# Kernel optimization log

Hardware: AMD Instinct MI355X
Metric: run time of the kernel (lower is better)

The kernel has to match this reference:

```python
import jax, jax.numpy as jnp
import numpy as np

CHUNK = 256
HEADS = 8  # kr
EPS = 1e-6


def setup_inputs() -> dict:
    key = jax.random.key(0)
    ks = jax.random.split(key, 8)
    B, S, D, V, K = 2, 4096, 1024, 32000, 128
    s = 0.02
    return {
        "x": jax.random.randint(ks[0], (B, S), 0, V),
        "emb_table": jax.random.normal(ks[1], (V, D), dtype=jnp.float32) * s,
        "Wq": jax.random.normal(ks[2], (D, K), dtype=jnp.float32) * s,
        "Wk": jax.random.normal(ks[3], (D, K), dtype=jnp.float32) * s,
        "Wv": jax.random.normal(ks[4], (D, D), dtype=jnp.float32) * s,
        "Wo": jax.random.normal(ks[5], (D, D), dtype=jnp.float32) * s,
        "ln_g": jnp.ones((D,), jnp.float32),
        "ln_b": jnp.zeros((D,), jnp.float32),
        "out_W": jax.random.normal(ks[6], (D, V), dtype=jnp.float32) * s,
        "out_b": jnp.zeros((V,), jnp.float32),
    }


def _forward(x, emb_table, Wq, Wk, Wv, Wo, ln_g, ln_b, out_W, out_b):
    B, S = x.shape
    D = emb_table.shape[1]
    K = Wq.shape[1]
    H, C = HEADS, CHUNK
    dk, dv = K // H, D // H
    nC = S // C

    emb = emb_table[x]                                   # [B,S,D]
    # build_causal_context: sum of emb shifted by 0..3
    ctx = emb
    for o in (1, 2, 3):
        ctx = ctx + jnp.pad(emb, ((0, 0), (o, 0), (0, 0)))[:, :S, :]

    phi = lambda t: jax.nn.elu(t) + 1.0                  # positive feature map
    q = phi(ctx @ Wq).reshape(B, nC, C, H, dk)
    k = phi(ctx @ Wk).reshape(B, nC, C, H, dk)
    v = (ctx @ Wv).reshape(B, nC, C, H, dv)
    xc = ctx.reshape(B, nC, C, D)

    qs, ks_, vs, xs = (jnp.moveaxis(a, 1, 0) for a in (q, k, v, xc))
    mask = jnp.tril(jnp.ones((C, C), bool))

    def step(carry, inp):
        S_st, S_t, bk, bv = carry                        # S_st:[B,H,dk,dv], S_t:[B,H,dk]
        qc, kc, vc, cc = inp
        # intra-chunk causal attention
        att = jnp.einsum('bchk,bshk->bhcs', qc, kc)
        att = jnp.where(mask[None, None], att, 0.0)
        num = jnp.einsum('bhcs,bshv->bchv', att, vc)
        # exact attention over previous chunk (bypass_kv)
        byp = jnp.einsum('bchk,bshk->bhcs', qc, bk)
        num = num + jnp.einsum('bhcs,bshv->bchv', byp, bv)
        # older chunks via outer-product state S_prev
        num = num + jnp.einsum('bchk,bhkv->bchv', qc, S_st)
        # denominator: running key-sum (S_time) + prev-chunk keys + causal cumsum
        kcum = jnp.cumsum(kc, axis=1)
        den = (jnp.einsum('bchk,bchk->bch', qc, kcum)
               + jnp.einsum('bchk,bhk->bch', qc, S_t + bk.sum(axis=1)))
        o = num / (den[..., None] + EPS)
        o = o.reshape(o.shape[0], C, D) @ Wo + cc        # out proj + residual
        # fold previous chunk into the long-range state, current chunk becomes bypass
        S_new = S_st + jnp.einsum('bshk,bshv->bhkv', bk, bv)
        St_new = S_t + bk.sum(axis=1)
        return (S_new, St_new, kc, vc), o

    init = (jnp.zeros((B, H, dk, dv), ctx.dtype),
            jnp.zeros((B, H, dk), ctx.dtype),
            jnp.zeros((B, C, H, dk), ctx.dtype),
            jnp.zeros((B, C, H, dv), ctx.dtype))
    _, outs = jax.lax.scan(step, init, (qs, ks_, vs, xs))
    out = jnp.moveaxis(outs, 0, 1).reshape(B, S, D)

    mu = out.mean(-1, keepdims=True)
    var = out.var(-1, keepdims=True)
    out = (out - mu) * jax.lax.rsqrt(var + 1e-5) * ln_g + ln_b
    return out @ out_W + out_b                           # [B,S,V] logits


def reference(x, emb_table, Wq, Wk, Wv, Wo, ln_g, ln_b, out_W, out_b):
    return _forward(x, emb_table, Wq, Wk, Wv, Wo, ln_g, ln_b, out_W, out_b)
```

## Files before the change

kernel.cpp:

```cpp
#include <hip/hip_runtime.h>
#include <hip/hip_bf16.h>

typedef __bf16 bf16_t;
typedef __bf16 bf16x4 __attribute__((ext_vector_type(4)));
typedef __bf16 bf16x8 __attribute__((ext_vector_type(8)));
typedef float f32x4 __attribute__((ext_vector_type(4)));

#define BB 2
#define SS 4096
#define DD 1024
#define VV 32000
#define HH 8
#define CC 256
#define NC 16

#define GLD_LDS16(gp, lp) __builtin_amdgcn_global_load_lds( \
    (const __attribute__((address_space(1))) void*)(gp),    \
    (__attribute__((address_space(3))) void*)(lp), 16, 0, 0)

__global__ __launch_bounds__(256) void ctx_kernel(
    const int* __restrict__ x, const float* __restrict__ emb,
    bf16_t* __restrict__ ctxb)
{
  const int row = blockIdx.x;
  const int b = row >> 12, s = row & (SS - 1);
  const int t = threadIdx.x;
  float4 a = make_float4(0.f, 0.f, 0.f, 0.f);
  #pragma unroll
  for (int o = 0; o < 4; ++o) {
    if (s - o >= 0) {
      const int idx = x[b * SS + s - o];
      const float4 e = *(const float4*)(emb + (size_t)idx * DD + t * 4);
      a.x += e.x; a.y += e.y; a.z += e.z; a.w += e.w;
    }
  }
  bf16x4 bv;
  bv[0] = (__bf16)a.x; bv[1] = (__bf16)a.y; bv[2] = (__bf16)a.z; bv[3] = (__bf16)a.w;
  *(bf16x4*)(ctxb + (size_t)row * DD + t * 4) = bv;
}

__global__ __launch_bounds__(256) void transpose_cvt(
    const float* __restrict__ src, bf16_t* __restrict__ dst,
    int srcRows, int srcCols)
{
  __shared__ __align__(16) float tile[128][65];
  const int c0 = blockIdx.x * 64, r0 = blockIdx.y * 128;
  const int t = threadIdx.x;
  #pragma unroll
  for (int p = 0; p < 8; ++p) {
    const int r = p * 16 + (t >> 4);
    const int c = (t & 15) * 4;
    *(float4*)&tile[r][c] = *(const float4*)(src + (size_t)(r0 + r) * srcCols + c0 + c);
  }
  __syncthreads();
  #pragma unroll
  for (int p = 0; p < 4; ++p) {
    const int j = p * 16 + (t >> 4);
    const int i0 = (t & 15) * 8;
    bf16x8 v;
    #pragma unroll
    for (int e = 0; e < 8; ++e) v[e] = (__bf16)tile[i0 + e][j];
    *(bf16x8*)(dst + (size_t)(c0 + j) * srcRows + r0 + i0) = v;
  }
}

template<int EPI>
__global__ __launch_bounds__(256, 4) void gemm128_kernel(
    const bf16_t* __restrict__ A, const bf16_t* __restrict__ BT,
    float* __restrict__ C, bf16_t* __restrict__ Cb,
    const float* __restrict__ extraF, const bf16_t* __restrict__ extraB,
    bf16_t* __restrict__ qb, bf16_t* __restrict__ kbx, bf16_t* __restrict__ vtb,
    int N, int K)
{
  __shared__ __align__(16) bf16_t As[128 * 64];
  __shared__ __align__(16) bf16_t Bs[128 * 64];
  const int bid = blockIdx.x;
  const int i = bid >> 3, xcd = bid & 7;
  const int by = xcd * 8 + (i & 7);
  const int bx = i >> 3;
  const int n0 = bx * 128, m0 = by * 128;
  const int t = threadIdx.x;
  const int w = t >> 6, lane = t & 63;
  const int wm = (w >> 1) * 64, wn = (w & 1) * 64;
  const int lr = lane & 15, lq = lane >> 4;
  f32x4 acc[4][4] = {};

  for (int k0 = 0; k0 < K; k0 += 64) {
    #pragma unroll
    for (int j = 0; j < 4; ++j) {
      const int idx = j * 256 + t;
      const int r = idx >> 3;
      const int sc = ((idx & 7) ^ (r & 7)) * 8;
      GLD_LDS16(A  + (size_t)(m0 + r) * K + k0 + sc, As + (size_t)idx * 8);
      GLD_LDS16(BT + (size_t)(n0 + r) * K + k0 + sc, Bs + (size_t)idx * 8);
    }
    asm volatile("s_waitcnt vmcnt(0)" ::: "memory");
    __syncthreads();
    bf16x8 af[4][2], bfr[4][2];
    #pragma unroll
    for (int ii = 0; ii < 4; ++ii) {
      const int ra = wm + ii * 16 + lr;
      const int rb = wn + ii * 16 + lr;
      #pragma unroll
      for (int ks = 0; ks < 2; ++ks) {
        const int col = ((ks * 4 + lq) ^ (lr & 7)) * 8;
        af[ii][ks]  = *(const bf16x8*)(As + ra * 64 + col);
        bfr[ii][ks] = *(const bf16x8*)(Bs + rb * 64 + col);
      }
    }
    #pragma unroll
    for (int mi = 0; mi < 4; ++mi)
      #pragma unroll
      for (int ni = 0; ni < 4; ++ni) {
        acc[mi][ni] = __builtin_amdgcn_mfma_f32_16x16x32_bf16(af[mi][0], bfr[ni][0], acc[mi][ni], 0, 0, 0);
        acc[mi][ni] = __builtin_amdgcn_mfma_f32_16x16x32_bf16(af[mi][1], bfr[ni][1], acc[mi][ni], 0, 0, 0);
      }
    __syncthreads();
  }

  if (EPI == 3) {
    #pragma unroll
    for (int mi = 0; mi < 4; ++mi) {
      const int row0 = m0 + wm + mi * 16 + lq * 4;
      #pragma unroll
      for (int ni = 0; ni < 4; ++ni) {
        const int col = n0 + wn + ni * 16 + lr;
        if (col < 256) {
          #pragma unroll
          for (int r = 0; r < 4; ++r) {
            float v = acc[mi][ni][r];
            v = v > 0.f ? v + 1.f : __expf(v);
            if (col < 128) qb [(size_t)(row0 + r) * 128 + col      ] = (__bf16)v;
            else           kbx[(size_t)(row0 + r) * 128 + col - 128] = (__bf16)v;
          }
        } else {
          const int vcol = col - 256;
          const int hh = vcol >> 7, dv = vcol & 127;
          const int bb = row0 >> 12, s0 = row0 & (SS - 1);
          bf16x4 pv;
          #pragma unroll
          for (int r = 0; r < 4; ++r) pv[r] = (__bf16)acc[mi][ni][r];
          *(bf16x4*)(vtb + ((size_t)((bb * HH + hh) * 128 + dv)) * SS + s0) = pv;
        }
      }
    }
    return;
  }
  #pragma unroll
  for (int mi = 0; mi < 4; ++mi) {
    #pragma unroll
    for (int r = 0; r < 4; ++r) {
      const int row = m0 + wm + mi * 16 + lq * 4 + r;
      #pragma unroll
      for (int ni = 0; ni < 4; ++ni) {
        const int col = n0 + wn + ni * 16 + lr;
        float v = acc[mi][ni][r];
        if (EPI == 1) {
          v += extraF[col];
          __builtin_nontemporal_store(v, &C[(size_t)row * N + col]);
        }
        if (EPI == 2) {
          v += (float)extraB[(size_t)row * N + col];
          Cb[(size_t)row * N + col] = (__bf16)v;
        }
      }
    }
  }
}

__global__ __launch_bounds__(64) void gstate_kernel(
    const bf16_t* __restrict__ kb, const bf16_t* __restrict__ vT,
    float* __restrict__ G, float* __restrict__ KS)
{
  const int bid = blockIdx.x;
  const int h = bid & 7, c = (bid >> 3) & 15, b = bid >> 7;
  const int lane = threadIdx.x;
  const int lr = lane & 15, lq = lane >> 4;
  __shared__ __align__(16) bf16_t ktl[16][264];
  for (int ss = 0; ss < 4; ++ss) {
    const int s = ss * 64 + lane;
    const bf16_t* src = kb + (size_t)(b * SS + c * CC + s) * 128 + h * 16;
    const bf16x8 v0 = *(const bf16x8*)src;
    const bf16x8 v1 = *(const bf16x8*)(src + 8);
    #pragma unroll
    for (int ii = 0; ii < 8; ++ii) { ktl[ii][s] = v0[ii]; ktl[8 + ii][s] = v1[ii]; }
  }
  __syncthreads();
  if (lane < 16) {
    float ks = 0.f;
    for (int s = 0; s < 256; ++s) ks += (float)ktl[lane][s];
    KS[((size_t)((b * NC + c) * HH + h)) * 16 + lane] = ks;
  }
  bf16x8 af[8];
  #pragma unroll
  for (int sk = 0; sk < 8; ++sk)
    af[sk] = *(const bf16x8*)&ktl[lr][sk * 32 + lq * 8];
  float* gout = G + ((size_t)((b * NC + c) * HH + h)) * 2048;
  #pragma unroll
  for (int nf = 0; nf < 8; ++nf) {
    f32x4 acc = {0.f, 0.f, 0.f, 0.f};
    #pragma unroll
    for (int sk = 0; sk < 8; ++sk) {
      const bf16x8 vb = *(const bf16x8*)(vT +
          ((size_t)((b * HH + h) * 128 + nf * 16 + lr)) * SS + c * CC + sk * 32 + lq * 8);
      acc = __builtin_amdgcn_mfma_f32_16x16x32_bf16(af[sk], vb, acc, 0, 0, 0);
    }
    #pragma unroll
    for (int r = 0; r < 4; ++r)
      gout[(size_t)(lq * 4 + r) * 128 + nf * 16 + lr] = acc[r];
  }
}

__global__ __launch_bounds__(512, 2) void attn_kernel(
    const bf16_t* __restrict__ qb, const bf16_t* __restrict__ kb,
    const bf16_t* __restrict__ vT, const float* __restrict__ Gb,
    const float* __restrict__ KS, bf16_t* __restrict__ outp)
{
  const int bid = blockIdx.x;
  const int h = bid & 7, c = (bid >> 3) & 15, b = bid >> 7;
  const int t = threadIdx.x;
  const int w = t >> 6, lane = t & 63;
  const int lr = lane & 15, lq = lane >> 4;
  const int rowbase = b * SS + c * CC;

  __shared__ __align__(16) bf16_t q_lds[256][24];
  __shared__ __align__(16) bf16_t k_lds[512][24];
  __shared__ __align__(16) bf16_t vt_lds[128][72];
  __shared__ __align__(16) bf16_t p_lds[8][32][72];
  __shared__ float s_f32[16][128];
  __shared__ float z_lds[16];
  __shared__ float dstate[256];

  if (t < 256) {
    const bf16_t* src = qb + (size_t)(rowbase + t) * 128 + h * 16;
    *(uint4*)&q_lds[t][0] = *(const uint4*)src;
    *(uint4*)&q_lds[t][8] = *(const uint4*)(src + 8);
  }
  {
    if (t < 256 && c == 0) {
      const uint4 z = {0u, 0u, 0u, 0u};
      *(uint4*)&k_lds[t][0] = z; *(uint4*)&k_lds[t][8] = z;
    } else {
      const int sg = (t < 256) ? (c - 1) * CC + t : c * CC + (t - 256);
      const bf16_t* src = kb + (size_t)(b * SS + sg) * 128 + h * 16;
      *(uint4*)&k_lds[t][0] = *(const uint4*)src;
      *(uint4*)&k_lds[t][8] = *(const uint4*)(src + 8);
    }
  }
  if (t < 16) {
    float z = 0.f;
    for (int j = 0; j + 2 <= c; ++j) z += KS[((size_t)((b * NC + j) * HH + h)) * 16 + t];
    z_lds[t] = z;
  }
  if (c >= 2) {
    for (int idx = t; idx < 2048; idx += 512) {
      float sv = 0.f;
      for (int j = 0; j + 2 <= c; ++j)
        sv += Gb[((size_t)((b * NC + j) * HH + h)) * 2048 + idx];
      ((float*)s_f32)[idx] = sv;
    }
  }
  __syncthreads();
  if (t < 256) {
    float d = 0.f;
    #pragma unroll
    for (int ii = 0; ii < 16; ++ii) d += (float)q_lds[t][ii] * z_lds[ii];
    dstate[t] = d;
  }

  const int wrow = w * 32;
  bf16x8 qf[2];
  #pragma unroll
  for (int mi = 0; mi < 2; ++mi) {
    bf16x8 v = {};
    if (lq < 2) v = *(const bf16x8*)&q_lds[wrow + mi * 16 + lr][lq * 8];
    qf[mi] = v;
  }
  f32x4 acc[2][8] = {};
  float den_l[2][4] = {};
  const int nc0 = (c == 0) ? 4 : 0;

  for (int nc = nc0; nc < 8; ++nc) {
    __syncthreads();
    {
      const int dv = t >> 2, kk = (t & 3) * 16;
      const int key0 = nc * 64;
      const int sg = (key0 < 256) ? (c - 1) * CC + key0 : c * CC + key0 - 256;
      const bf16_t* src = vT + ((size_t)((b * HH + h) * 128 + dv)) * SS + sg + kk;
      *(uint4*)&vt_lds[dv][kk]     = *(const uint4*)src;
      *(uint4*)&vt_lds[dv][kk + 8] = *(const uint4*)(src + 8);
    }
    __syncthreads();
    f32x4 attf[2][4];
    #pragma unroll
    for (int nf = 0; nf < 4; ++nf) {
      bf16x8 kv = {};
      if (lq < 2) kv = *(const bf16x8*)&k_lds[nc * 64 + nf * 16 + lr][lq * 8];
      #pragma unroll
      for (int mi = 0; mi < 2; ++mi) {
        const f32x4 zero = {0.f, 0.f, 0.f, 0.f};
        attf[mi][nf] = __builtin_amdgcn_mfma_f32_16x16x32_bf16(qf[mi], kv, zero, 0, 0, 0);
      }
    }
    #pragma unroll
    for (int mi = 0; mi < 2; ++mi)
      #pragma unroll
      for (int nf = 0; nf < 4; ++nf)
        #pragma unroll
        for (int r = 0; r < 4; ++r) {
          const int row_l = wrow + mi * 16 + lq * 4 + r;
          const int key_l = nc * 64 + nf * 16 + lr;
          float a = attf[mi][nf][r];
          if (key_l >= 256 && key_l - 256 > row_l) a = 0.f;
          den_l[mi][r] += a;
          p_lds[w][mi * 16 + lq * 4 + r][nf * 16 + lr] = (__bf16)a;
        }
    #pragma unroll
    for (int ks = 0; ks < 2; ++ks) {
      bf16x8 pa[2];
      #pragma unroll
      for (int mi = 0; mi < 2; ++mi)
        pa[mi] = *(const bf16x8*)&p_lds[w][mi * 16 + lr][ks * 32 + lq * 8];
      #pragma unroll
      for (int nf = 0; nf < 8; ++nf) {
        const bf16x8 vb = *(const bf16x8*)&vt_lds[nf * 16 + lr][ks * 32 + lq * 8];
        #pragma unroll
        for (int mi = 0; mi < 2; ++mi)
          acc[mi][nf] = __builtin_amdgcn_mfma_f32_16x16x32_bf16(pa[mi], vb, acc[mi][nf], 0, 0, 0);
      }
    }
  }

  if (c >= 2) {
    #pragma unroll
    for (int mi = 0; mi < 2; ++mi)
      for (int r = 0; r < 4; ++r) {
        const int row_l = wrow + mi * 16 + lq * 4 + r;
        float qrow[16];
        #pragma unroll
        for (int ii = 0; ii < 16; ++ii) qrow[ii] = (float)q_lds[row_l][ii];
        #pragma unroll
        for (int nf = 0; nf < 8; ++nf) {
          float sacc = 0.f;
          #pragma unroll
          for (int ii = 0; ii < 16; ++ii) sacc += qrow[ii] * s_f32[ii][nf * 16 + lr];
          acc[mi][nf][r] += sacc;
        }
      }
  }
  #pragma unroll
  for (int mi = 0; mi < 2; ++mi)
    #pragma unroll
    for (int r = 0; r < 4; ++r) {
      float d = den_l[mi][r];
      d += __shfl_xor(d, 1, 64); d += __shfl_xor(d, 2, 64);
      d += __shfl_xor(d, 4, 64); d += __shfl_xor(d, 8, 64);
      const int row_l = wrow + mi * 16 + lq * 4 + r;
      den_l[mi][r] = 1.0f / (d + dstate[row_l] + 1e-6f);
    }
  #pragma unroll
  for (int mi = 0; mi < 2; ++mi)
    #pragma unroll
    for (int r = 0; r < 4; ++r) {
      const size_t row_g = rowbase + wrow + mi * 16 + lq * 4 + r;
      const float inv = den_l[mi][r];
      #pragma unroll
      for (int nf = 0; nf < 8; ++nf)
        outp[row_g * DD + h * 128 + nf * 16 + lr] = (__bf16)(acc[mi][nf][r] * inv);
    }
}

__global__ __launch_bounds__(256) void ln_kernel(
    const bf16_t* __restrict__ hb, const float* __restrict__ g,
    const float* __restrict__ bta, bf16_t* __restrict__ out)
{
  const int row = blockIdx.x;
  const int t = threadIdx.x;
  const bf16x4 xb = *(const bf16x4*)(hb + (size_t)row * DD + t * 4);
  float4 x = make_float4((float)xb[0], (float)xb[1], (float)xb[2], (float)xb[3]);
  float s  = x.x + x.y + x.z + x.w;
  float s2 = x.x*x.x + x.y*x.y + x.z*x.z + x.w*x.w;
  #pragma unroll
  for (int off = 32; off > 0; off >>= 1) {
    s  += __shfl_down(s,  off, 64);
    s2 += __shfl_down(s2, off, 64);
  }
  __shared__ float ws[8];
  if ((t & 63) == 0) { ws[(t >> 6) * 2] = s; ws[(t >> 6) * 2 + 1] = s2; }
  __syncthreads();
  const float ts  = ws[0] + ws[2] + ws[4] + ws[6];
  const float ts2 = ws[1] + ws[3] + ws[5] + ws[7];
  const float mu  = ts * (1.0f / DD);
  const float var = ts2 * (1.0f / DD) - mu * mu;
  const float inv = rsqrtf(var + 1e-5f);
  const float4 gv = ((const float4*)g)[t];
  const float4 bv = ((const float4*)bta)[t];
  bf16x4 o;
  o[0] = (__bf16)((x.x - mu) * inv * gv.x + bv.x);
  o[1] = (__bf16)((x.y - mu) * inv * gv.y + bv.y);
  o[2] = (__bf16)((x.z - mu) * inv * gv.z + bv.z);
  o[3] = (__bf16)((x.w - mu) * inv * gv.w + bv.w);
  *(bf16x4*)(out + (size_t)row * DD + t * 4) = o;
}

extern "C" void kernel_launch(void* const* d_in, const int* in_sizes, int n_in,
                              void* d_out, int out_size, void* d_ws, size_t ws_size,
                              hipStream_t stream) {
  (void)in_sizes; (void)n_in; (void)out_size; (void)ws_size;
  const int*   x    = (const int*)d_in[0];
  const float* emb  = (const float*)d_in[1];
  const float* Wq   = (const float*)d_in[2];
  const float* Wk   = (const float*)d_in[3];
  const float* Wv   = (const float*)d_in[4];
  const float* Wo   = (const float*)d_in[5];
  const float* ln_g = (const float*)d_in[6];
  const float* ln_b = (const float*)d_in[7];
  const float* outW = (const float*)d_in[8];
  const float* outb = (const float*)d_in[9];
  float* out = (float*)d_out;

  char* ws = (char*)d_ws;
  bf16_t* ctx_bf  = (bf16_t*)(ws + 0);
  bf16_t* qbuf    = (bf16_t*)(ws + 16777216ull);
  bf16_t* kbuf    = (bf16_t*)(ws + 18874368ull);
  bf16_t* vTbuf   = (bf16_t*)(ws + 20971520ull);
  bf16_t* attn_bf = (bf16_t*)(ws + 37748736ull);
  bf16_t* h_pre   = (bf16_t*)(ws + 54525952ull);
  float*  Gbuf    = (float*) (ws + 71303168ull);
  float*  KSbuf   = (float*) (ws + 73400320ull);
  bf16_t* WqkvT   = (bf16_t*)(ws + 73416704ull);
  bf16_t* WoT     = (bf16_t*)(ws + 76038144ull);
  bf16_t* outWT   = (bf16_t*)(ws + 78135296ull);
  bf16_t* h_bf    = attn_bf;

  transpose_cvt<<<dim3(2, 8),   256, 0, stream>>>(Wq,   WqkvT,             DD, 128);
  transpose_cvt<<<dim3(2, 8),   256, 0, stream>>>(Wk,   WqkvT + 128 * DD,  DD, 128);
  transpose_cvt<<<dim3(16, 8),  256, 0, stream>>>(Wv,   WqkvT + 256 * DD,  DD, DD);
  transpose_cvt<<<dim3(16, 8),  256, 0, stream>>>(Wo,   WoT,               DD, DD);
  transpose_cvt<<<dim3(500, 8), 256, 0, stream>>>(outW, outWT,             DD, VV);

  ctx_kernel<<<BB * SS, 256, 0, stream>>>(x, emb, ctx_bf);

  gemm128_kernel<3><<<(1280 / 128) * (BB * SS / 128), 256, 0, stream>>>(
      ctx_bf, WqkvT, nullptr, nullptr, nullptr, nullptr, qbuf, kbuf, vTbuf, 1280, DD);

  gstate_kernel<<<BB * NC * HH, 64, 0, stream>>>(kbuf, vTbuf, Gbuf, KSbuf);
  attn_kernel<<<BB * NC * HH, 512, 0, stream>>>(qbuf, kbuf, vTbuf, Gbuf, KSbuf, attn_bf);

  gemm128_kernel<2><<<(DD / 128) * (BB * SS / 128), 256, 0, stream>>>(
      attn_bf, WoT, nullptr, h_pre, nullptr, ctx_bf, nullptr, nullptr, nullptr, DD, DD);

  ln_kernel<<<BB * SS, 256, 0, stream>>>(h_pre, ln_g, ln_b, h_bf);

  gemm128_kernel<1><<<(VV / 128) * (BB * SS / 128), 256, 0, stream>>>(
      h_bf, outWT, out, nullptr, outb, nullptr, nullptr, nullptr, nullptr, VV, DD);
}
```

Measured before the change: 787.7 us.

## Make GEMM persistent over N tiles and prefetch next K-slice during MFMA

The GEMM kernel becomes persistent along N: each block owns one M tile and loops over N tiles with stride LANES, and the launch grid shrinks to 64*LANES blocks (1024 for the vocab projection). Fragments are read into registers, then the next K slice, or the first slice of the next N tile, is issued into LDS before the MFMAs run, so global loads overlap compute with a single LDS buffer. The intent is to hide load latency and cut block launch overhead. The cost is fewer resident blocks and possible tail imbalance, since 250 N tiles do not split evenly over 16 lanes.

```diff
diff --git a/kernel.cpp b/kernel.cpp
--- a/kernel.cpp
+++ b/kernel.cpp
@@ -64,104 +64,113 @@
   }
 }
 
+#define STAGE(N0S, K0S) do {                                                  \
+  _Pragma("unroll") for (int j = 0; j < 4; ++j) {                             \
+    const int idx = j * 256 + t;                                              \
+    const int r = idx >> 3;                                                   \
+    const int sc = ((idx & 7) ^ (r & 7)) * 8;                                 \
+    GLD_LDS16(A  + (size_t)(m0 + r) * K + (K0S) + sc, As + (size_t)idx * 8);  \
+    GLD_LDS16(BT + (size_t)((N0S) + r) * K + (K0S) + sc, Bs + (size_t)idx * 8); \
+  } } while (0)
+
 template<int EPI>
 __global__ __launch_bounds__(256, 4) void gemm128_kernel(
     const bf16_t* __restrict__ A, const bf16_t* __restrict__ BT,
     float* __restrict__ C, bf16_t* __restrict__ Cb,
     const float* __restrict__ extraF, const bf16_t* __restrict__ extraB,
     bf16_t* __restrict__ qb, bf16_t* __restrict__ kbx, bf16_t* __restrict__ vtb,
-    int N, int K)
+    int N, int K, int LANES)
 {
   __shared__ __align__(16) bf16_t As[128 * 64];
   __shared__ __align__(16) bf16_t Bs[128 * 64];
   const int bid = blockIdx.x;
-  const int i = bid >> 3, xcd = bid & 7;
-  const int by = xcd * 8 + (i & 7);
-  const int bx = i >> 3;
-  const int n0 = bx * 128, m0 = by * 128;
+  const int xcd = bid & 7, sl = (bid >> 3) & 7, lane16 = bid >> 6;
+  const int by = xcd * 8 + sl;
+  const int m0 = by * 128;
+  const int NBX = N >> 7;
   const int t = threadIdx.x;
   const int w = t >> 6, lane = t & 63;
   const int wm = (w >> 1) * 64, wn = (w & 1) * 64;
   const int lr = lane & 15, lq = lane >> 4;
-  f32x4 acc[4][4] = {};
-
-  for (int k0 = 0; k0 < K; k0 += 64) {
-    #pragma unroll
-    for (int j = 0; j < 4; ++j) {
-      const int idx = j * 256 + t;
-      const int r = idx >> 3;
-      const int sc = ((idx & 7) ^ (r & 7)) * 8;
-      GLD_LDS16(A  + (size_t)(m0 + r) * K + k0 + sc, As + (size_t)idx * 8);
-      GLD_LDS16(BT + (size_t)(n0 + r) * K + k0 + sc, Bs + (size_t)idx * 8);
-    }
-    asm volatile("s_waitcnt vmcnt(0)" ::: "memory");
-    __syncthreads();
-    bf16x8 af[4][2], bfr[4][2];
-    #pragma unroll
-    for (int ii = 0; ii < 4; ++ii) {
-      const int ra = wm + ii * 16 + lr;
-      const int rb = wn + ii * 16 + lr;
-      #pragma unroll
-      for (int ks = 0; ks < 2; ++ks) {
-        const int col = ((ks * 4 + lq) ^ (lr & 7)) * 8;
-        af[ii][ks]  = *(const bf16x8*)(As + ra * 64 + col);
-        bfr[ii][ks] = *(const bf16x8*)(Bs + rb * 64 + col);
-      }
-    }
-    #pragma unroll
-    for (int mi = 0; mi < 4; ++mi)
-      #pragma unroll
-      for (int ni = 0; ni < 4; ++ni) {
-        acc[mi][ni] = __builtin_amdgcn_mfma_f32_16x16x32_bf16(af[mi][0], bfr[ni][0], acc[mi][ni], 0, 0, 0);
-        acc[mi][ni] = __builtin_amdgcn_mfma_f32_16x16x32_bf16(af[mi][1], bfr[ni][1], acc[mi][ni], 0, 0, 0);
-      }
-    __syncthreads();
-  }
-
-  if (EPI == 3) {
-    #pragma unroll
-    for (int mi = 0; mi < 4; ++mi) {
-      const int row0 = m0 + wm + mi * 16 + lq * 4;
-      #pragma unroll
-      for (int ni = 0; ni < 4; ++ni) {
-        const int col = n0 + wn + ni * 16 + lr;
-        if (col < 256) {
+
+  STAGE(lane16 * 128, 0);
+
+  for (int bx = lane16; bx < NBX; bx += LANES) {
+    const int n0 = bx * 128;
+    f32x4 acc[4][4] = {};
+    for (int k0 = 0; k0 < K; k0 += 64) {
+      asm volatile("s_waitcnt vmcnt(0)" ::: "memory");
+      __syncthreads();
+      bf16x8 af[4][2], bfr[4][2];
+      #pragma unroll
+      for (int ii = 0; ii < 4; ++ii) {
+        const int ra = wm + ii * 16 + lr;
+        const int rb = wn + ii * 16 + lr;
+        #pragma unroll
+        for (int ks = 0; ks < 2; ++ks) {
+          const int col = ((ks * 4 + lq) ^ (lr & 7)) * 8;
+          af[ii][ks]  = *(const bf16x8*)(As + ra * 64 + col);
+          bfr[ii][ks] = *(const bf16x8*)(Bs + rb * 64 + col);
+        }
+      }
+      __syncthreads();
+      const int k1 = k0 + 64;
+      if (k1 < K)                STAGE(n0, k1);
+      else if (bx + LANES < NBX) STAGE((bx + LANES) * 128, 0);
+      #pragma unroll
+      for (int mi = 0; mi < 4; ++mi)
+        #pragma unroll
+        for (int ni = 0; ni < 4; ++ni) {
+          acc[mi][ni] = __builtin_amdgcn_mfma_f32_16x16x32_bf16(af[mi][0], bfr[ni][0], acc[mi][ni], 0, 0, 0);
+          acc[mi][ni] = __builtin_amdgcn_mfma_f32_16x16x32_bf16(af[mi][1], bfr[ni][1], acc[mi][ni], 0, 0, 0);
+        }
+    }
+
+    if (EPI == 3) {
+      #pragma unroll
+      for (int mi = 0; mi < 4; ++mi) {
+        const int row0 = m0 + wm + mi * 16 + lq * 4;
+        #pragma unroll
+        for (int ni = 0; ni < 4; ++ni) {
+          const int col = n0 + wn + ni * 16 + lr;
+          if (col < 256) {
+            #pragma unroll
+            for (int r = 0; r < 4; ++r) {
+              float v = acc[mi][ni][r];
+              v = v > 0.f ? v + 1.f : __expf(v);
+              if (col < 128) qb [(size_t)(row0 + r) * 128 + col      ] = (__bf16)v;
+              else           kbx[(size_t)(row0 + r) * 128 + col - 128] = (__bf16)v;
+            }
+          } else {
+            const int vcol = col - 256;
+            const int hh = vcol >> 7, dv = vcol & 127;
+            const int bb = row0 >> 12, s0 = row0 & (SS - 1);
+            bf16x4 pv;
+            #pragma unroll
+            for (int r = 0; r < 4; ++r) pv[r] = (__bf16)acc[mi][ni][r];
+            *(bf16x4*)(vtb + ((size_t)((bb * HH + hh) * 128 + dv)) * SS + s0) = pv;
+          }
+        }
+      }
+    } else {
+      #pragma unroll
+      for (int mi = 0; mi < 4; ++mi) {
+        #pragma unroll
+        for (int r = 0; r < 4; ++r) {
+          const int row = m0 + wm + mi * 16 + lq * 4 + r;
           #pragma unroll
-          for (int r = 0; r < 4; ++r) {
+          for (int ni = 0; ni < 4; ++ni) {
+            const int col = n0 + wn + ni * 16 + lr;
             float v = acc[mi][ni][r];
-            v = v > 0.f ? v + 1.f : __expf(v);
-            if (col < 128) qb [(size_t)(row0 + r) * 128 + col      ] = (__bf16)v;
-            else           kbx[(size_t)(row0 + r) * 128 + col - 128] = (__bf16)v;
+            if (EPI == 1) {
+              v += extraF[col];
+              __builtin_nontemporal_store(v, &C[(size_t)row * N + col]);
+            }
+            if (EPI == 2) {
+              v += (float)extraB[(size_t)row * N + col];
+              Cb[(size_t)row * N + col] = (__bf16)v;
+            }
           }
-        } else {
-          const int vcol = col - 256;
-          const int hh = vcol >> 7, dv = vcol & 127;
-          const int bb = row0 >> 12, s0 = row0 & (SS - 1);
-          bf16x4 pv;
-          #pragma unroll
-          for (int r = 0; r < 4; ++r) pv[r] = (__bf16)acc[mi][ni][r];
-          *(bf16x4*)(vtb + ((size_t)((bb * HH + hh) * 128 + dv)) * SS + s0) = pv;
-        }
-      }
-    }
-    return;
-  }
-  #pragma unroll
-  for (int mi = 0; mi < 4; ++mi) {
-    #pragma unroll
-    for (int r = 0; r < 4; ++r) {
-      const int row = m0 + wm + mi * 16 + lq * 4 + r;
-      #pragma unroll
-      for (int ni = 0; ni < 4; ++ni) {
-        const int col = n0 + wn + ni * 16 + lr;
-        float v = acc[mi][ni][r];
-        if (EPI == 1) {
-          v += extraF[col];
-          __builtin_nontemporal_store(v, &C[(size_t)row * N + col]);
-        }
-        if (EPI == 2) {
-          v += (float)extraB[(size_t)row * N + col];
-          Cb[(size_t)row * N + col] = (__bf16)v;
         }
       }
     }
@@ -441,17 +450,17 @@
 
   ctx_kernel<<<BB * SS, 256, 0, stream>>>(x, emb, ctx_bf);
 
-  gemm128_kernel<3><<<(1280 / 128) * (BB * SS / 128), 256, 0, stream>>>(
-      ctx_bf, WqkvT, nullptr, nullptr, nullptr, nullptr, qbuf, kbuf, vTbuf, 1280, DD);
+  gemm128_kernel<3><<<64 * 10, 256, 0, stream>>>(
+      ctx_bf, WqkvT, nullptr, nullptr, nullptr, nullptr, qbuf, kbuf, vTbuf, 1280, DD, 10);
 
   gstate_kernel<<<BB * NC * HH, 64, 0, stream>>>(kbuf, vTbuf, Gbuf, KSbuf);
   attn_kernel<<<BB * NC * HH, 512, 0, stream>>>(qbuf, kbuf, vTbuf, Gbuf, KSbuf, attn_bf);
 
-  gemm128_kernel<2><<<(DD / 128) * (BB * SS / 128), 256, 0, stream>>>(
-      attn_bf, WoT, nullptr, h_pre, nullptr, ctx_bf, nullptr, nullptr, nullptr, DD, DD);
+  gemm128_kernel<2><<<64 * 8, 256, 0, stream>>>(
+      attn_bf, WoT, nullptr, h_pre, nullptr, ctx_bf, nullptr, nullptr, nullptr, DD, DD, 8);
 
   ln_kernel<<<BB * SS, 256, 0, stream>>>(h_pre, ln_g, ln_b, h_bf);
 
-  gemm128_kernel<1><<<(VV / 128) * (BB * SS / 128), 256, 0, stream>>>(
-      h_bf, outWT, out, nullptr, outb, nullptr, nullptr, nullptr, nullptr, VV, DD);
-}
+  gemm128_kernel<1><<<64 * 16, 256, 0, stream>>>(
+      h_bf, outWT, out, nullptr, outb, nullptr, nullptr, nullptr, nullptr, VV, DD, 16);
+}
```

Result: slower. 2.450 ms (+211.0%).
